# Kernel tuning notes

Hardware: AMD Instinct MI355X
Metric: run time of the kernel (lower is better)

Reference implementation:

```python
import jax, jax.numpy as jnp
import numpy as np

NF = 128  # latent_dim / number of filters


def setup_inputs() -> dict:
    key = jax.random.key(0)
    k1, k2, k3, k4 = jax.random.split(key, 4)
    B, H, W, C = 4, 64, 64, 128
    x = jax.random.normal(k1, (B, H, W, C), dtype=jnp.float32)
    y = jax.random.normal(k2, (B, H, W, C), dtype=jnp.float32)
    # 1x1 conv kernels (C_in, C_out) + biases, glorot-ish scale
    scale = 1.0 / np.sqrt(C)
    W1 = jax.random.normal(k3, (C, NF), dtype=jnp.float32) * scale
    W2 = jax.random.normal(k4, (C, NF), dtype=jnp.float32) * scale
    b1 = jnp.zeros((NF,), dtype=jnp.float32)
    b2 = jnp.zeros((NF,), dtype=jnp.float32)
    return {"x": x, "y": y, "W1": W1, "b1": b1, "W2": W2, "b2": b2}


def reference(x, y, W1, b1, W2, b2):
    B, H, Wd, C = x.shape
    hw = H * Wd
    # 1x1 convs == per-pixel matmul
    xq = jnp.einsum('bhwc,cf->bhwf', x, W1) + b1   # conv1(x)
    yk = jnp.einsum('bhwc,cf->bhwf', y, W2) + b2   # conv2(y)
    xq_r = xq.reshape(B, hw, NF)
    yk_r = yk.reshape(B, hw, NF)
    # A_ij = sigmoid(y_i . x_j), full (hw x hw) sigmoid attention
    A = jax.nn.sigmoid(jnp.einsum('bic,bjc->bij', yk_r, xq_r))
    out = jnp.einsum('bij,bjc->bic', A, yk_r).reshape(B, H, Wd, NF)
    # residual add of the *projected* x (matches original: x was overwritten by conv1)
    out = out + xq
    return out
```

## Files before the change

### kernel.cpp

```cpp
#include <hip/hip_runtime.h>
#include <hip/hip_bf16.h>
#include <stdint.h>

typedef float f32x16 __attribute__((ext_vector_type(16)));
typedef float f32x4  __attribute__((ext_vector_type(4)));
typedef short s16x8  __attribute__((ext_vector_type(8)));
typedef unsigned int u32x4 __attribute__((ext_vector_type(4)));

#define HWSZ   4096
#define NBATCH 4
#define LOG2E  1.44269504088896340736f

__device__ __forceinline__ unsigned short f2bf(float f) {
    unsigned u = __builtin_bit_cast(unsigned, f);
    u += 0x7FFFu + ((u >> 16) & 1u);
    return (unsigned short)(u >> 16);
}
__device__ __forceinline__ unsigned cvt_pk_bf16(float lo, float hi) {
    __hip_bfloat162 h = __float22bfloat162_rn(make_float2(lo, hi));
    return *reinterpret_cast<unsigned*>(&h);
}

__global__ __launch_bounds__(256, 1) void proj_kernel(
    const float* __restrict__ x, const float* __restrict__ y,
    const float* __restrict__ W1, const float* __restrict__ b1,
    const float* __restrict__ W2, const float* __restrict__ b2,
    float* __restrict__ xq_f32,
    unsigned short* __restrict__ xq_bf,
    unsigned short* __restrict__ yk_bf,
    unsigned short* __restrict__ ykT_bf)
{
    __shared__ unsigned short Xlds[64][136];
    __shared__ unsigned short Ylds[64][136];
    __shared__ unsigned short Tlds[128][72];

    const int t    = threadIdx.x;
    const int lane = t & 63;
    const int w    = t >> 6;
    const int l31  = lane & 31;
    const int g    = lane >> 5;
    const int r0   = blockIdx.x * 64;
    const int b    = r0 >> 12;
    const int j0   = r0 & (HWSZ - 1);

    #pragma unroll
    for (int i = 0; i < 8; ++i) {
        int li = t + 256 * i;
        int row = li >> 5, c = (li & 31) * 4;
        float4 vx = *(const float4*)(x + (size_t)(r0 + row) * 128 + c);
        float4 vy = *(const float4*)(y + (size_t)(r0 + row) * 128 + c);
        *(uint2*)&Xlds[row][c] = make_uint2(cvt_pk_bf16(vx.x, vx.y), cvt_pk_bf16(vx.z, vx.w));
        *(uint2*)&Ylds[row][c] = make_uint2(cvt_pk_bf16(vy.x, vy.y), cvt_pk_bf16(vy.z, vy.w));
    }
    __syncthreads();

    const int m  = w >> 1;
    const int fh = w & 1;
    const float* Wm = m ? W2 : W1;
    const float* bm = m ? b2 : b1;
    const unsigned short* A0 = m ? &Ylds[0][0] : &Xlds[0][0];

    f32x16 acc[2][2];
    #pragma unroll
    for (int i = 0; i < 16; ++i) {
        acc[0][0][i] = 0.f; acc[0][1][i] = 0.f;
        acc[1][0][i] = 0.f; acc[1][1][i] = 0.f;
    }

    #pragma unroll
    for (int ks = 0; ks < 8; ++ks) {
        s16x8 bfr[2];
        #pragma unroll
        for (int ft = 0; ft < 2; ++ft) {
            const float* wp = Wm + (size_t)(ks * 16 + g * 8) * 128 + fh * 64 + ft * 32 + l31;
            #pragma unroll
            for (int i = 0; i < 8; ++i)
                bfr[ft][i] = (short)f2bf(wp[(size_t)i * 128]);
        }
        #pragma unroll
        for (int rt = 0; rt < 2; ++rt) {
            s16x8 af = *(const s16x8*)(A0 + (size_t)(rt * 32 + l31) * 136 + ks * 16 + g * 8);
            acc[rt][0] = __builtin_amdgcn_mfma_f32_32x32x16_bf16(af, bfr[0], acc[rt][0], 0, 0, 0);
            acc[rt][1] = __builtin_amdgcn_mfma_f32_32x32x16_bf16(af, bfr[1], acc[rt][1], 0, 0, 0);
        }
    }

    const float bias_v[2] = { bm[fh * 64 + l31], bm[fh * 64 + 32 + l31] };

    if (m == 0) {
        #pragma unroll
        for (int rt = 0; rt < 2; ++rt)
        #pragma unroll
        for (int ft = 0; ft < 2; ++ft) {
            int f = fh * 64 + ft * 32 + l31;
            #pragma unroll
            for (int r = 0; r < 16; ++r) {
                int row = rt * 32 + (r & 3) + 8 * (r >> 2) + 4 * g;
                float v = acc[rt][ft][r] + bias_v[ft];
                size_t o = (size_t)(r0 + row) * 128 + f;
                xq_f32[o] = v;
                xq_bf[o]  = f2bf(v * LOG2E);
            }
        }
    } else {
        #pragma unroll
        for (int rt = 0; rt < 2; ++rt)
        #pragma unroll
        for (int ft = 0; ft < 2; ++ft) {
            int f = fh * 64 + ft * 32 + l31;
            #pragma unroll
            for (int rg = 0; rg < 4; ++rg) {
                float p0 = acc[rt][ft][4 * rg + 0] + bias_v[ft];
                float p1 = acc[rt][ft][4 * rg + 1] + bias_v[ft];
                float p2 = acc[rt][ft][4 * rg + 2] + bias_v[ft];
                float p3 = acc[rt][ft][4 * rg + 3] + bias_v[ft];
                int jb = rt * 32 + 8 * rg + 4 * g;
                *(uint2*)&Tlds[f][jb] = make_uint2(cvt_pk_bf16(p0, p1), cvt_pk_bf16(p2, p3));
                size_t o = (size_t)(r0 + jb) * 128 + f;
                yk_bf[o]       = f2bf(p0);
                yk_bf[o + 128] = f2bf(p1);
                yk_bf[o + 256] = f2bf(p2);
                yk_bf[o + 384] = f2bf(p3);
            }
        }
    }
    __syncthreads();

    {
        int f  = t >> 1;
        int jh = (t & 1) * 32;
        unsigned short* dst = ykT_bf + ((size_t)(b * 128 + f)) * HWSZ + j0 + jh;
        #pragma unroll
        for (int c = 0; c < 4; ++c)
            *(s16x8*)(dst + c * 8) = *(const s16x8*)&Tlds[f][jh + c * 8];
    }
}

#define KT_STR   136
#define VT_STR   72
#define KT_BYTES (64 * KT_STR * 2)
#define VT_BYTES (128 * VT_STR * 2)
#define BUF_BYTES (KT_BYTES + VT_BYTES)

template<bool SPLIT>
__global__ __launch_bounds__(256, 2) void attn_kernel(
    const unsigned short* __restrict__ Kbf,
    const unsigned short* __restrict__ Qbf,
    const unsigned short* __restrict__ Vtbf,
    const float* __restrict__ resid,
    float* __restrict__ outp)
{
    __shared__ __align__(16) char smem[2 * BUF_BYTES];

    const int t    = threadIdx.x;
    const int lane = t & 63;
    const int w    = t >> 6;
    const int qt   = w & 1;
    const int jt   = w >> 1;
    const int l31  = lane & 31;
    const int g    = lane >> 5;

    int bid = blockIdx.x;
    int half = 0;
    if (SPLIT) { half = bid >> 8; bid &= 255; }
    const int b      = bid >> 6;
    const int qb     = (bid & 63) * 64;
    const int jBegin = half * (HWSZ / 2);
    const int nt     = (SPLIT ? HWSZ / 2 : HWSZ) / 64;

    s16x8 qfrag[8];
    {
        const unsigned short* qp =
            Qbf + (((size_t)(b * HWSZ + qb + 32 * qt + l31)) << 7) + g * 8;
        #pragma unroll
        for (int fs = 0; fs < 8; ++fs)
            qfrag[fs] = *(const s16x8*)(qp + fs * 16);
    }

    f32x16 acc[4];
    #pragma unroll
    for (int ft = 0; ft < 4; ++ft)
        #pragma unroll
        for (int i = 0; i < 16; ++i) acc[ft][i] = 0.f;

    const unsigned short* Kbase = Kbf  + (((size_t)b * HWSZ) << 7);
    const unsigned short* Vbase = Vtbf + (((size_t)b) << 7) * HWSZ;

    const unsigned short* kSrc = Kbase + (size_t)(jBegin + (t >> 4)) * 128 + (t & 15) * 8;
    const unsigned short* vSrc = Vbase + (size_t)(t >> 3) * HWSZ + jBegin + (t & 7) * 8;
    const int kDst = (t >> 4) * KT_STR + (t & 15) * 8;
    const int vDst = (t >> 3) * VT_STR + (t & 7) * 8;

    {
        unsigned short* Kl = (unsigned short*)smem;
        unsigned short* Vl = (unsigned short*)(smem + KT_BYTES);
        #pragma unroll
        for (int i = 0; i < 4; ++i)
            *(s16x8*)(Kl + kDst + i * 16 * KT_STR) = *(const s16x8*)(kSrc + (size_t)i * 2048);
        #pragma unroll
        for (int i = 0; i < 4; ++i)
            *(s16x8*)(Vl + vDst + i * 32 * VT_STR) = *(const s16x8*)(vSrc + (size_t)i * 32 * HWSZ);
    }
    __syncthreads();

    int c = 0;
    for (int it = 0; it < nt; ++it) {
        const bool pre = (it + 1 < nt);
        s16x8 kr[4], vr[4];
        if (pre) {
            kSrc += 64 * 128;
            vSrc += 64;
            #pragma unroll
            for (int i = 0; i < 4; ++i)
                kr[i] = *(const s16x8*)(kSrc + (size_t)i * 2048);
            #pragma unroll
            for (int i = 0; i < 4; ++i)
                vr[i] = *(const s16x8*)(vSrc + (size_t)i * 32 * HWSZ);
        }

        const unsigned short* Kl = (const unsigned short*)(smem + c * BUF_BYTES);
        const unsigned short* Vl = (const unsigned short*)(smem + c * BUF_BYTES + KT_BYTES);

        f32x16 sa, sb;
        #pragma unroll
        for (int i = 0; i < 16; ++i) { sa[i] = 0.f; sb[i] = 0.f; }
        const unsigned short* Krow = Kl + (size_t)(32 * jt + l31) * KT_STR + g * 8;
        __builtin_amdgcn_s_setprio(1);
        #pragma unroll
        for (int fs = 0; fs < 4; ++fs) {
            sa = __builtin_amdgcn_mfma_f32_32x32x16_bf16(
                     *(const s16x8*)(Krow + fs * 16), qfrag[fs], sa, 0, 0, 0);
            sb = __builtin_amdgcn_mfma_f32_32x32x16_bf16(
                     *(const s16x8*)(Krow + (fs + 4) * 16), qfrag[fs + 4], sb, 0, 0, 0);
        }
        __builtin_amdgcn_s_setprio(0);

        unsigned W0[4], W1[4];
        #pragma unroll
        for (int rg = 0; rg < 4; ++rg) {
            float s0 = sa[4 * rg + 0] + sb[4 * rg + 0];
            float s1 = sa[4 * rg + 1] + sb[4 * rg + 1];
            float s2 = sa[4 * rg + 2] + sb[4 * rg + 2];
            float s3 = sa[4 * rg + 3] + sb[4 * rg + 3];
            float p0 = __builtin_amdgcn_rcpf(1.f + __builtin_amdgcn_exp2f(-s0));
            float p1 = __builtin_amdgcn_rcpf(1.f + __builtin_amdgcn_exp2f(-s1));
            float p2 = __builtin_amdgcn_rcpf(1.f + __builtin_amdgcn_exp2f(-s2));
            float p3 = __builtin_amdgcn_rcpf(1.f + __builtin_amdgcn_exp2f(-s3));
            W0[rg] = cvt_pk_bf16(p0, p1);
            W1[rg] = cvt_pk_bf16(p2, p3);
        }

        #pragma unroll
        for (int s2 = 0; s2 < 2; ++s2) {
            unsigned o0 = g ? W0[2 * s2 + 1] : W0[2 * s2];
            unsigned o1 = g ? W1[2 * s2 + 1] : W1[2 * s2];
            unsigned t0 = g ? W0[2 * s2]     : W0[2 * s2 + 1];
            unsigned t1 = g ? W1[2 * s2]     : W1[2 * s2 + 1];
            unsigned r0 = __shfl_xor(t0, 32, 64);
            unsigned r1 = __shfl_xor(t1, 32, 64);
            u32x4 pw;
            pw[0] = g ? r0 : o0;
            pw[1] = g ? r1 : o1;
            pw[2] = g ? o0 : r0;
            pw[3] = g ? o1 : r1;
            s16x8 pf = __builtin_bit_cast(s16x8, pw);
            const int ks = 2 * jt + s2;
            __builtin_amdgcn_s_setprio(1);
            #pragma unroll
            for (int ft = 0; ft < 4; ++ft) {
                s16x8 vf = *(const s16x8*)(Vl + (size_t)(32 * ft + l31) * VT_STR + ks * 16 + g * 8);
                acc[ft] = __builtin_amdgcn_mfma_f32_32x32x16_bf16(pf, vf, acc[ft], 0, 0, 0);
            }
            __builtin_amdgcn_s_setprio(0);
        }

        if (pre) {
            unsigned short* Kd = (unsigned short*)(smem + (c ^ 1) * BUF_BYTES);
            unsigned short* Vd = (unsigned short*)(smem + (c ^ 1) * BUF_BYTES + KT_BYTES);
            #pragma unroll
            for (int i = 0; i < 4; ++i)
                *(s16x8*)(Kd + kDst + i * 16 * KT_STR) = kr[i];
            #pragma unroll
            for (int i = 0; i < 4; ++i)
                *(s16x8*)(Vd + vDst + i * 32 * VT_STR) = vr[i];
        }
        __syncthreads();
        c ^= 1;
    }

    float* red = (float*)smem;
    if (jt == 1) {
        #pragma unroll
        for (int ft = 0; ft < 4; ++ft)
        #pragma unroll
        for (int r = 0; r < 16; ++r) {
            int row = (r & 3) + 8 * (r >> 2) + 4 * g;
            red[qt * 4096 + row * 128 + 32 * ft + l31] = acc[ft][r];
        }
    }
    __syncthreads();
    if (jt == 0) {
        float* op = outp + (SPLIT ? (size_t)half * ((size_t)NBATCH * HWSZ * 128) : 0);
        #pragma unroll
        for (int ft = 0; ft < 4; ++ft)
        #pragma unroll
        for (int r = 0; r < 16; ++r) {
            int row = (r & 3) + 8 * (r >> 2) + 4 * g;
            float v = acc[ft][r] + red[qt * 4096 + row * 128 + 32 * ft + l31];
            int q = qb + 32 * qt + row;
            size_t o = (((size_t)(b * HWSZ + q)) << 7) + 32 * ft + l31;
            if (SPLIT) op[o] = v;
            else       op[o] = v + resid[o];
        }
    }
}

__global__ __launch_bounds__(256, 1) void reduce_kernel(
    const float* __restrict__ p0, const float* __restrict__ p1, float* outp)
{
    int i = blockIdx.x * 256 + threadIdx.x;
    f32x4 a = ((const f32x4*)p0)[i];
    f32x4 b = ((const f32x4*)p1)[i];
    f32x4 c = ((f32x4*)outp)[i];
    ((f32x4*)outp)[i] = a + b + c;
}

extern "C" void kernel_launch(void* const* d_in, const int* in_sizes, int n_in,
                              void* d_out, int out_size, void* d_ws, size_t ws_size,
                              hipStream_t stream) {
    const float* x  = (const float*)d_in[0];
    const float* y  = (const float*)d_in[1];
    const float* W1 = (const float*)d_in[2];
    const float* b1 = (const float*)d_in[3];
    const float* W2 = (const float*)d_in[4];
    const float* b2 = (const float*)d_in[5];
    float* out = (float*)d_out;

    const size_t NELEM = (size_t)NBATCH * HWSZ * 128;
    unsigned short* xq_bf  = (unsigned short*)d_ws;
    unsigned short* yk_bf  = xq_bf + NELEM;
    unsigned short* ykT_bf = yk_bf + NELEM;
    float* part = (float*)(ykT_bf + NELEM);
    const bool split = ws_size >= (NELEM * 2 * 3 + NELEM * 4 * 2);

    proj_kernel<<<(int)(NBATCH * HWSZ / 64), 256, 0, stream>>>(
        x, y, W1, b1, W2, b2, out, xq_bf, yk_bf, ykT_bf);

    if (split) {
        attn_kernel<true><<<512, 256, 0, stream>>>(xq_bf, yk_bf, ykT_bf, out, part);
        reduce_kernel<<<(int)(NELEM / 1024), 256, 0, stream>>>(part, part + NELEM, out);
    } else {
        attn_kernel<false><<<256, 256, 0, stream>>>(xq_bf, yk_bf, ykT_bf, out, out);
    }
}
```

Before: 75.37 us.

## Add 128-query-tile attention kernel with 4-way key split and reduction

Adds an attention kernel where each block handles 128 queries (one 32-row tile per wave) over a quarter of the key range, with double-buffered K/V tiles in LDS. Each K/V tile is reused across four query tiles instead of splitting keys within the block, which removes the in-block cross-wave reduction. The partials go to four workspace buffers, and a new 4-way reduce kernel sums them with the residual. The trade-off is more workspace traffic and larger partial buffers to write and read. The new path runs only when the workspace is large enough.

```diff
diff --git a/kernel.cpp b/kernel.cpp
--- a/kernel.cpp
+++ b/kernel.cpp
@@ -142,6 +142,162 @@
 #define VT_BYTES (128 * VT_STR * 2)
 #define BUF_BYTES (KT_BYTES + VT_BYTES)
 
+__global__ __launch_bounds__(256, 2) void attn128_kernel(
+    const unsigned short* __restrict__ Kbf,
+    const unsigned short* __restrict__ Qbf,
+    const unsigned short* __restrict__ Vtbf,
+    float* __restrict__ outp)
+{
+    __shared__ __align__(16) char smem[2 * BUF_BYTES];
+
+    const int t    = threadIdx.x;
+    const int lane = t & 63;
+    const int qt   = t >> 6;
+    const int l31  = lane & 31;
+    const int g    = lane >> 5;
+
+    const int split = blockIdx.x >> 7;
+    const int r     = blockIdx.x & 127;
+    const int b     = r >> 5;
+    const int qb    = (r & 31) * 128;
+    const int jBegin = split * (HWSZ / 4);
+    const int nt     = (HWSZ / 4) / 64;
+
+    s16x8 qfrag[8];
+    {
+        const unsigned short* qp =
+            Qbf + (((size_t)(b * HWSZ + qb + 32 * qt + l31)) << 7) + g * 8;
+        #pragma unroll
+        for (int fs = 0; fs < 8; ++fs)
+            qfrag[fs] = *(const s16x8*)(qp + fs * 16);
+    }
+
+    f32x16 acc[4];
+    #pragma unroll
+    for (int ft = 0; ft < 4; ++ft)
+        #pragma unroll
+        for (int i = 0; i < 16; ++i) acc[ft][i] = 0.f;
+
+    const unsigned short* Kbase = Kbf  + (((size_t)b * HWSZ) << 7);
+    const unsigned short* Vbase = Vtbf + (((size_t)b) << 7) * HWSZ;
+
+    const unsigned short* kSrc = Kbase + (size_t)(jBegin + (t >> 4)) * 128 + (t & 15) * 8;
+    const unsigned short* vSrc = Vbase + (size_t)(t >> 3) * HWSZ + jBegin + (t & 7) * 8;
+    const int kDst = (t >> 4) * KT_STR + (t & 15) * 8;
+    const int vDst = (t >> 3) * VT_STR + (t & 7) * 8;
+
+    {
+        unsigned short* Kl = (unsigned short*)smem;
+        unsigned short* Vl = (unsigned short*)(smem + KT_BYTES);
+        #pragma unroll
+        for (int i = 0; i < 4; ++i)
+            *(s16x8*)(Kl + kDst + i * 16 * KT_STR) = *(const s16x8*)(kSrc + (size_t)i * 2048);
+        #pragma unroll
+        for (int i = 0; i < 4; ++i)
+            *(s16x8*)(Vl + vDst + i * 32 * VT_STR) = *(const s16x8*)(vSrc + (size_t)i * 32 * HWSZ);
+    }
+    __syncthreads();
+
+    int c = 0;
+    for (int it = 0; it < nt; ++it) {
+        const bool pre = (it + 1 < nt);
+        s16x8 kr[4], vr[4];
+        if (pre) {
+            kSrc += 64 * 128;
+            vSrc += 64;
+            #pragma unroll
+            for (int i = 0; i < 4; ++i)
+                kr[i] = *(const s16x8*)(kSrc + (size_t)i * 2048);
+            #pragma unroll
+            for (int i = 0; i < 4; ++i)
+                vr[i] = *(const s16x8*)(vSrc + (size_t)i * 32 * HWSZ);
+        }
+
+        const unsigned short* Kl = (const unsigned short*)(smem + c * BUF_BYTES);
+        const unsigned short* Vl = (const unsigned short*)(smem + c * BUF_BYTES + KT_BYTES);
+
+        #pragma unroll
+        for (int jt = 0; jt < 2; ++jt) {
+            f32x16 sa, sb;
+            #pragma unroll
+            for (int i = 0; i < 16; ++i) { sa[i] = 0.f; sb[i] = 0.f; }
+            const unsigned short* Krow = Kl + (size_t)(32 * jt + l31) * KT_STR + g * 8;
+            __builtin_amdgcn_s_setprio(1);
+            #pragma unroll
+            for (int fs = 0; fs < 4; ++fs) {
+                sa = __builtin_amdgcn_mfma_f32_32x32x16_bf16(
+                         *(const s16x8*)(Krow + fs * 16), qfrag[fs], sa, 0, 0, 0);
+                sb = __builtin_amdgcn_mfma_f32_32x32x16_bf16(
+                         *(const s16x8*)(Krow + (fs + 4) * 16), qfrag[fs + 4], sb, 0, 0, 0);
+            }
+            __builtin_amdgcn_s_setprio(0);
+
+            unsigned W0[4], W1[4];
+            #pragma unroll
+            for (int rg = 0; rg < 4; ++rg) {
+                float s0 = sa[4 * rg + 0] + sb[4 * rg + 0];
+                float s1 = sa[4 * rg + 1] + sb[4 * rg + 1];
+                float s2v = sa[4 * rg + 2] + sb[4 * rg + 2];
+                float s3 = sa[4 * rg + 3] + sb[4 * rg + 3];
+                float p0 = __builtin_amdgcn_rcpf(1.f + __builtin_amdgcn_exp2f(-s0));
+                float p1 = __builtin_amdgcn_rcpf(1.f + __builtin_amdgcn_exp2f(-s1));
+                float p2 = __builtin_amdgcn_rcpf(1.f + __builtin_amdgcn_exp2f(-s2v));
+                float p3 = __builtin_amdgcn_rcpf(1.f + __builtin_amdgcn_exp2f(-s3));
+                W0[rg] = cvt_pk_bf16(p0, p1);
+                W1[rg] = cvt_pk_bf16(p2, p3);
+            }
+
+            #pragma unroll
+            for (int s2 = 0; s2 < 2; ++s2) {
+                unsigned o0 = g ? W0[2 * s2 + 1] : W0[2 * s2];
+                unsigned o1 = g ? W1[2 * s2 + 1] : W1[2 * s2];
+                unsigned t0 = g ? W0[2 * s2]     : W0[2 * s2 + 1];
+                unsigned t1 = g ? W1[2 * s2]     : W1[2 * s2 + 1];
+                unsigned r0 = __shfl_xor(t0, 32, 64);
+                unsigned r1 = __shfl_xor(t1, 32, 64);
+                u32x4 pw;
+                pw[0] = g ? r0 : o0;
+                pw[1] = g ? r1 : o1;
+                pw[2] = g ? o0 : r0;
+                pw[3] = g ? o1 : r1;
+                s16x8 pf = __builtin_bit_cast(s16x8, pw);
+                const int ks = 2 * jt + s2;
+                __builtin_amdgcn_s_setprio(1);
+                #pragma unroll
+                for (int ft = 0; ft < 4; ++ft) {
+                    s16x8 vf = *(const s16x8*)(Vl + (size_t)(32 * ft + l31) * VT_STR + ks * 16 + g * 8);
+                    acc[ft] = __builtin_amdgcn_mfma_f32_32x32x16_bf16(pf, vf, acc[ft], 0, 0, 0);
+                }
+                __builtin_amdgcn_s_setprio(0);
+            }
+        }
+
+        if (pre) {
+            unsigned short* Kd = (unsigned short*)(smem + (c ^ 1) * BUF_BYTES);
+            unsigned short* Vd = (unsigned short*)(smem + (c ^ 1) * BUF_BYTES + KT_BYTES);
+            #pragma unroll
+            for (int i = 0; i < 4; ++i)
+                *(s16x8*)(Kd + kDst + i * 16 * KT_STR) = kr[i];
+            #pragma unroll
+            for (int i = 0; i < 4; ++i)
+                *(s16x8*)(Vd + vDst + i * 32 * VT_STR) = vr[i];
+        }
+        __syncthreads();
+        c ^= 1;
+    }
+
+    float* op = outp + (size_t)split * ((size_t)NBATCH * HWSZ * 128);
+    #pragma unroll
+    for (int ft = 0; ft < 4; ++ft)
+    #pragma unroll
+    for (int r2 = 0; r2 < 16; ++r2) {
+        int row = (r2 & 3) + 8 * (r2 >> 2) + 4 * g;
+        int q = qb + 32 * qt + row;
+        size_t o = (((size_t)(b * HWSZ + q)) << 7) + 32 * ft + l31;
+        op[o] = acc[ft][r2];
+    }
+}
+
 template<bool SPLIT>
 __global__ __launch_bounds__(256, 2) void attn_kernel(
     const unsigned short* __restrict__ Kbf,
@@ -240,11 +396,11 @@
         for (int rg = 0; rg < 4; ++rg) {
             float s0 = sa[4 * rg + 0] + sb[4 * rg + 0];
             float s1 = sa[4 * rg + 1] + sb[4 * rg + 1];
-            float s2 = sa[4 * rg + 2] + sb[4 * rg + 2];
+            float s2v = sa[4 * rg + 2] + sb[4 * rg + 2];
             float s3 = sa[4 * rg + 3] + sb[4 * rg + 3];
             float p0 = __builtin_amdgcn_rcpf(1.f + __builtin_amdgcn_exp2f(-s0));
             float p1 = __builtin_amdgcn_rcpf(1.f + __builtin_amdgcn_exp2f(-s1));
-            float p2 = __builtin_amdgcn_rcpf(1.f + __builtin_amdgcn_exp2f(-s2));
+            float p2 = __builtin_amdgcn_rcpf(1.f + __builtin_amdgcn_exp2f(-s2v));
             float p3 = __builtin_amdgcn_rcpf(1.f + __builtin_amdgcn_exp2f(-s3));
             W0[rg] = cvt_pk_bf16(p0, p1);
             W1[rg] = cvt_pk_bf16(p2, p3);
@@ -315,7 +471,7 @@
     }
 }
 
-__global__ __launch_bounds__(256, 1) void reduce_kernel(
+__global__ __launch_bounds__(256, 1) void reduce2_kernel(
     const float* __restrict__ p0, const float* __restrict__ p1, float* outp)
 {
     int i = blockIdx.x * 256 + threadIdx.x;
@@ -323,6 +479,19 @@
     f32x4 b = ((const f32x4*)p1)[i];
     f32x4 c = ((f32x4*)outp)[i];
     ((f32x4*)outp)[i] = a + b + c;
+}
+
+__global__ __launch_bounds__(256, 1) void reduce4_kernel(
+    const float* __restrict__ parts, float* __restrict__ outp)
+{
+    const size_t NELEM4 = (size_t)NBATCH * HWSZ * 128 / 4;
+    size_t i = (size_t)blockIdx.x * 256 + threadIdx.x;
+    f32x4 a = ((const f32x4*)parts)[i];
+    f32x4 b = ((const f32x4*)parts)[i + NELEM4];
+    f32x4 c = ((const f32x4*)parts)[i + 2 * NELEM4];
+    f32x4 d = ((const f32x4*)parts)[i + 3 * NELEM4];
+    f32x4 e = ((f32x4*)outp)[i];
+    ((f32x4*)outp)[i] = (a + b) + (c + d) + e;
 }
 
 extern "C" void kernel_launch(void* const* d_in, const int* in_sizes, int n_in,
@@ -341,14 +510,16 @@
     unsigned short* yk_bf  = xq_bf + NELEM;
     unsigned short* ykT_bf = yk_bf + NELEM;
     float* part = (float*)(ykT_bf + NELEM);
-    const bool split = ws_size >= (NELEM * 2 * 3 + NELEM * 4 * 2);
 
     proj_kernel<<<(int)(NBATCH * HWSZ / 64), 256, 0, stream>>>(
         x, y, W1, b1, W2, b2, out, xq_bf, yk_bf, ykT_bf);
 
-    if (split) {
+    if (ws_size >= NELEM * (6 + 16)) {
+        attn128_kernel<<<512, 256, 0, stream>>>(xq_bf, yk_bf, ykT_bf, part);
+        reduce4_kernel<<<(int)(NELEM / 1024), 256, 0, stream>>>(part, out);
+    } else if (ws_size >= NELEM * (6 + 8)) {
         attn_kernel<true><<<512, 256, 0, stream>>>(xq_bf, yk_bf, ykT_bf, out, part);
-        reduce_kernel<<<(int)(NELEM / 1024), 256, 0, stream>>>(part, part + NELEM, out);
+        reduce2_kernel<<<(int)(NELEM / 1024), 256, 0, stream>>>(part, part + NELEM, out);
     } else {
         attn_kernel<false><<<256, 256, 0, stream>>>(xq_bf, yk_bf, ykT_bf, out, out);
     }
```

Measured after the change: 70.68 us. -6.2%, faster.
